# Kernel tuning notes

Hardware: AMD Instinct MI355X
Metric: run time of the kernel (lower is better)

## Reference

```python
import jax, jax.numpy as jnp
import numpy as np
import math

D_MODEL = 512
N_HEAD = 8
HEAD_DIM = D_MODEL // N_HEAD


def _rel_sinusoid(seq_len, dim):
    # Sinusoidal embedding for relative positions -seq_len .. seq_len-1, shape [2L, dim]
    half = dim // 2
    inv_freq = jnp.exp(jnp.arange(half, dtype=jnp.float32) * (-math.log(10000.0) / (half - 1)))
    ang = jnp.arange(-seq_len, seq_len, dtype=jnp.float32)[:, None] * inv_freq[None, :]
    return jnp.concatenate([jnp.sin(ang), jnp.cos(ang)], axis=1)  # [2L, dim]


def _shift(BD):
    # Transformer-XL shift trick: [b, n, L, 2L] -> [b, n, L, L]
    b, n, L, _ = BD.shape
    BD = jnp.concatenate([BD, jnp.zeros((b, n, L, 1), BD.dtype)], axis=-1)  # [b,n,L,2L+1]
    BD = BD.reshape(b, n, -1, L)[:, :, :-1].reshape(b, n, L, -1)  # [b,n,L,2L]
    return BD[:, :, :, L:]


def setup_inputs() -> dict:
    key = jax.random.key(0)
    ks = jax.random.split(key, 6)
    B, L = 8, 1024
    x = jax.random.normal(ks[0], (B, L, D_MODEL), jnp.float32)
    mask = jax.random.randint(ks[1], (B, L), 0, 2).astype(jnp.int32)
    W_qkv = jax.random.normal(ks[2], (D_MODEL, 3 * D_MODEL), jnp.float32) / math.sqrt(D_MODEL)
    r_r_bias = jax.random.normal(ks[3], (N_HEAD, HEAD_DIM), jnp.float32) * 0.1
    r_w_bias = jax.random.normal(ks[4], (N_HEAD, HEAD_DIM), jnp.float32) * 0.1
    w_kr = jax.random.normal(ks[5], (HEAD_DIM, HEAD_DIM), jnp.float32) * 0.1
    return {"x": x, "mask": mask, "W_qkv": W_qkv, "r_r_bias": r_r_bias, "r_w_bias": r_w_bias, "w_kr": w_kr}


def reference(x, mask, W_qkv, r_r_bias, r_w_bias, w_kr):
    B, L, d_model = x.shape
    scale = math.sqrt(HEAD_DIM)
    pos_embed = _rel_sinusoid(L, HEAD_DIM)  # [2L, head_dim]

    qkv = x @ W_qkv  # [B, L, 3*d_model]
    q, k, v = jnp.split(qkv, 3, axis=-1)
    q = q.reshape(B, L, N_HEAD, HEAD_DIM).transpose(0, 2, 1, 3)  # [B, H, L, hd]
    k = k.reshape(B, L, N_HEAD, HEAD_DIM).transpose(0, 2, 1, 3)
    v = v.reshape(B, L, N_HEAD, HEAD_DIM).transpose(0, 2, 1, 3)

    rw_head_q = q + r_r_bias[None, :, None, :]
    AC = jnp.einsum('bnqd,bnkd->bnqk', rw_head_q, k)  # [B,H,L,L]

    rel = pos_embed @ w_kr  # [2L, hd]
    D_ = jnp.einsum('nd,ld->nl', r_w_bias, rel)[None, :, None, :]  # [1,H,1,2L]
    B_ = jnp.einsum('bnqd,ld->bnql', q, rel)  # [B,H,L,2L]
    BD = _shift(B_ + D_)  # [B,H,L,L]

    attn = (AC + BD) / scale
    attn = jnp.where(mask[:, None, None, :] == 0, jnp.float32(1e-9), attn)
    attn = jax.nn.softmax(attn, axis=-1)  # dropout is identity at eval

    out = jnp.einsum('bnqk,bnkd->bnqd', attn, v)  # [B,H,L,hd]
    return out.transpose(0, 2, 1, 3).reshape(B, L, d_model)
```

## Files before the change

### kernel.cpp

```cpp
#include <hip/hip_runtime.h>
#include <hip/hip_bf16.h>
#include <stdint.h>

typedef __bf16 bf16x8 __attribute__((ext_vector_type(8)));
typedef float  f32x4  __attribute__((ext_vector_type(4)));

#define D_MODEL 512
#define N_HEAD  8
#define HD      64
#define L_      1024
#define SCALE   0.125f
#define EXP_NEG8 3.35462628e-4f
#define L2E     1.44269504f
#define NEG8L2E -11.54156036f

__device__ __forceinline__ unsigned short f2bf(float f) {
  unsigned int u = __builtin_bit_cast(unsigned int, f);
  u += 0x7FFFu + ((u >> 16) & 1u);
  return (unsigned short)(u >> 16);
}
__device__ __forceinline__ float bf2f(unsigned short h) {
  unsigned int u = ((unsigned int)h) << 16;
  return __builtin_bit_cast(float, u);
}

__device__ __forceinline__ void gld_lds16(const void* g, void* l) {
  __builtin_amdgcn_global_load_lds(
      (const __attribute__((address_space(1))) void*)g,
      (__attribute__((address_space(3))) void*)l, 16, 0, 0);
}
__device__ __forceinline__ void gld_lds4(const void* g, void* l) {
  __builtin_amdgcn_global_load_lds(
      (const __attribute__((address_space(1))) void*)g,
      (__attribute__((address_space(3))) void*)l, 4, 0, 0);
}

__global__ __launch_bounds__(256) void k_cvt_x(const float* __restrict__ x,
                                               unsigned short* __restrict__ xbf) {
  int t = blockIdx.x * 256 + threadIdx.x;
  const float4* p = reinterpret_cast<const float4*>(x) + (size_t)t * 2;
  float4 a = p[0], b = p[1];
  ushort4 o0 = { f2bf(a.x), f2bf(a.y), f2bf(a.z), f2bf(a.w) };
  ushort4 o1 = { f2bf(b.x), f2bf(b.y), f2bf(b.z), f2bf(b.w) };
  ushort4* q = reinterpret_cast<ushort4*>(xbf) + (size_t)t * 2;
  q[0] = o0; q[1] = o1;
}

__global__ __launch_bounds__(256) void k_cvt_wt(const float* __restrict__ W,
                                                unsigned short* __restrict__ Wt) {
  __shared__ float tile[32][33];
  int kb = blockIdx.x;
  int nb = blockIdx.y;
  int t = threadIdx.x;
  int r = t >> 3, c4 = (t & 7) * 4;
  float4 v = *reinterpret_cast<const float4*>(W + (size_t)(kb * 32 + r) * 1536 + nb * 32 + c4);
  tile[r][c4 + 0] = v.x; tile[r][c4 + 1] = v.y; tile[r][c4 + 2] = v.z; tile[r][c4 + 3] = v.w;
  __syncthreads();
  int a = t >> 3, b4 = (t & 7) * 4;
  ushort4 o = { f2bf(tile[b4 + 0][a]), f2bf(tile[b4 + 1][a]),
                f2bf(tile[b4 + 2][a]), f2bf(tile[b4 + 3][a]) };
  *reinterpret_cast<ushort4*>(Wt + (size_t)(nb * 32 + a) * 512 + kb * 32 + b4) = o;
}

__global__ __launch_bounds__(256) void k_stab(float* __restrict__ SCF,
                                              unsigned short* __restrict__ SBF) {
  int tid = blockIdx.x * 256 + threadIdx.x;
  int l = tid >> 6, d = tid & 63;
  const float kInv = -9.210340371976184f / 31.0f;
  float f = expf((float)(d & 31) * kInv);
  float ang = (float)l * f;
  float v = (d < 32) ? sinf(ang) : cosf(ang);
  SCF[tid] = v;
  SBF[tid] = f2bf(v);
}

__global__ __launch_bounds__(256) void k_wz(const unsigned short* __restrict__ Wt,
                                            const float* __restrict__ wkr,
                                            const float* __restrict__ rwb,
                                            unsigned short* __restrict__ Wzt,
                                            float* __restrict__ CZ) {
  __shared__ float wkrS[64][64];
  __shared__ float panS[64][36];
  int blk = blockIdx.x;
  int h = blk >> 4, kc = blk & 15;
  int t = threadIdx.x;
  for (int i = t; i < 4096; i += 256) wkrS[i >> 6][i & 63] = wkr[i];
  {
    int d = t >> 2, j0 = (t & 3) * 8;
    const unsigned short* src = Wt + (size_t)(h * 64 + d) * 512 + kc * 32 + j0;
    for (int j = 0; j < 8; ++j) panS[d][j0 + j] = bf2f(src[j]);
  }
  __syncthreads();
  int e = t >> 2, j0 = (t & 3) * 8;
  float acc[8];
  for (int j = 0; j < 8; ++j) acc[j] = 0.f;
  for (int d = 0; d < 64; ++d) {
    float wv = wkrS[e][d];
    for (int j = 0; j < 8; ++j) acc[j] += wv * panS[d][j0 + j];
  }
  unsigned short* dst = Wzt + (size_t)(h * 64 + e) * 512 + kc * 32 + j0;
  ushort4 o0 = { f2bf(acc[0]), f2bf(acc[1]), f2bf(acc[2]), f2bf(acc[3]) };
  ushort4 o1 = { f2bf(acc[4]), f2bf(acc[5]), f2bf(acc[6]), f2bf(acc[7]) };
  *reinterpret_cast<ushort4*>(dst) = o0;
  *reinterpret_cast<ushort4*>(dst + 4) = o1;
  if (kc == 0 && t < 64) {
    float c = 0.f;
    for (int d = 0; d < 64; ++d) c += wkrS[t][d] * rwb[h * 64 + d];
    CZ[h * 64 + t] = c;
  }
}

__global__ __launch_bounds__(256, 3) void k_gemm_qkv(const unsigned short* __restrict__ Xbf,
                                                     const unsigned short* __restrict__ Wt,
                                                     const float* __restrict__ rrb,
                                                     const float* __restrict__ SCF,
                                                     const float* __restrict__ CZ,
                                                     unsigned short* __restrict__ QKV,
                                                     unsigned short* __restrict__ Vt,
                                                     unsigned short* __restrict__ Aq) {
  __shared__ unsigned short As[2][128][32];
  __shared__ unsigned short Bs[2][128][32];
  int lin = blockIdx.y * 64 + blockIdx.x;
  int xcd = lin & 7, idx = lin >> 3;
  int bx = xcd * 8 + idx / 16;
  int by = idx % 16;
  int m0 = bx * 128;
  int n0 = by * 128;
  int w = threadIdx.x >> 6, lane = threadIdx.x & 63;
  int lr = lane & 15, g = lane >> 4;
  int wm = (w >> 1) * 64, wn = (w & 1) * 64;
  int srow = lane >> 2, schk = (lane & 3) * 8;

  auto stage = [&](int buf, int k0) {
#pragma unroll
    for (int j = 0; j < 2; ++j) {
      int row = w * 32 + j * 16 + srow;
      gld_lds16(Xbf + (size_t)(m0 + row) * 512 + k0 + schk, &As[buf][w * 32 + j * 16][0]);
      gld_lds16(Wt  + (size_t)(n0 + row) * 512 + k0 + schk, &Bs[buf][w * 32 + j * 16][0]);
    }
  };

  f32x4 acc[4][4];
  for (int i = 0; i < 4; ++i) for (int j = 0; j < 4; ++j) acc[i][j] = (f32x4){0.f, 0.f, 0.f, 0.f};

  stage(0, 0);
  __syncthreads();

  for (int it = 0; it < 16; ++it) {
    int cur = it & 1;
    if (it < 15) stage(cur ^ 1, (it + 1) * 32);
    bf16x8 a[4], b[4];
#pragma unroll
    for (int mt = 0; mt < 4; ++mt)
      a[mt] = __builtin_bit_cast(bf16x8, *reinterpret_cast<const uint4*>(&As[cur][wm + mt * 16 + lr][g * 8]));
#pragma unroll
    for (int nt = 0; nt < 4; ++nt)
      b[nt] = __builtin_bit_cast(bf16x8, *reinterpret_cast<const uint4*>(&Bs[cur][wn + nt * 16 + lr][g * 8]));
#pragma unroll
    for (int mt = 0; mt < 4; ++mt)
#pragma unroll
      for (int nt = 0; nt < 4; ++nt)
        acc[mt][nt] = __builtin_amdgcn_mfma_f32_16x16x32_bf16(a[mt], b[nt], acc[mt][nt], 0, 0, 0);
    __syncthreads();
  }

  int region = n0 >> 9;
  if (region == 3) {
    int nvb = (n0 - 1536) + wn;
    int h = nvb >> 6;
    int bb = m0 >> 10;
    float cz0 = CZ[nvb + lr];
    float cz1 = CZ[nvb + 16 + lr];
    float cz2 = CZ[nvb + 32 + lr];
    float cz3 = CZ[nvb + 48 + lr];
#pragma unroll
    for (int mt = 0; mt < 4; ++mt)
#pragma unroll
      for (int r = 0; r < 4; ++r) {
        int m = m0 + wm + mt * 16 + g * 4 + r;
        int lrow = m & 1023;
        const float* sc = SCF + (size_t)lrow * 64;
        float s0 = sc[lr], s1 = sc[16 + lr], c0 = sc[32 + lr], c1 = sc[48 + lr];
        float z0 = acc[mt][0][r] + cz0;
        float z1 = acc[mt][1][r] + cz1;
        float z2 = acc[mt][2][r] + cz2;
        float z3 = acc[mt][3][r] + cz3;
        unsigned short* ap = Aq + ((size_t)(bb * 8 + h) * 1024 + lrow) * 64;
        ap[lr]      = f2bf((z0 * c0 + z2 * s0) * SCALE);
        ap[16 + lr] = f2bf((z1 * c1 + z3 * s1) * SCALE);
        ap[32 + lr] = f2bf((z2 * c0 - z0 * s0) * SCALE);
        ap[48 + lr] = f2bf((z3 * c1 - z1 * s1) * SCALE);
      }
  } else if (region == 2) {
#pragma unroll
    for (int mt = 0; mt < 4; ++mt)
#pragma unroll
      for (int nt = 0; nt < 4; ++nt) {
        int m = m0 + wm + mt * 16 + g * 4;
        int n = n0 + wn + nt * 16 + lr;
        int nv = n - 1024;
        int bb = m >> 10, h = nv >> 6, d = nv & 63;
        ushort4 o = { f2bf(acc[mt][nt][0]), f2bf(acc[mt][nt][1]),
                      f2bf(acc[mt][nt][2]), f2bf(acc[mt][nt][3]) };
        *reinterpret_cast<ushort4*>(Vt + (size_t)((bb * 8 + h) * 64 + d) * 1024 + (m & 1023)) = o;
      }
  } else if (region == 0) {
#pragma unroll
    for (int mt = 0; mt < 4; ++mt)
#pragma unroll
      for (int nt = 0; nt < 4; ++nt) {
        int n = n0 + wn + nt * 16 + lr;
        float bias = rrb[n];
#pragma unroll
        for (int r = 0; r < 4; ++r) {
          int m = m0 + wm + mt * 16 + g * 4 + r;
          QKV[(size_t)m * 1536 + n] = f2bf((acc[mt][nt][r] + bias) * SCALE);
        }
      }
  } else {
#pragma unroll
    for (int mt = 0; mt < 4; ++mt)
#pragma unroll
      for (int nt = 0; nt < 4; ++nt)
#pragma unroll
        for (int r = 0; r < 4; ++r) {
          int m = m0 + wm + mt * 16 + g * 4 + r;
          int n = n0 + wn + nt * 16 + lr;
          QKV[(size_t)m * 1536 + n] = f2bf(acc[mt][nt][r]);
        }
  }
}

__global__ __launch_bounds__(256, 3) void k_attn(const unsigned short* __restrict__ QKV,
                                                 const unsigned short* __restrict__ Vt,
                                                 const unsigned short* __restrict__ Sbf,
                                                 const unsigned short* __restrict__ Aq,
                                                 const int* __restrict__ mask,
                                                 float* __restrict__ out) {
  __shared__ unsigned short KtS[2][64][64];
  __shared__ unsigned short VtS[2][64][64];
  __shared__ int MtS[2][64];
  __shared__ unsigned short pS[4][32][64];

  int n_ = blockIdx.x;
  int l = (n_ & 7) * 64 + (n_ >> 3);
  int bh = l >> 3, qt = l & 7;
  int b = bh >> 3, h = bh & 7;
  int w = threadIdx.x >> 6, lane = threadIdx.x & 63;
  int lr = lane & 15, g = lane >> 4;
  int qw0 = qt * 128 + w * 32;
  int rsub = lane >> 3;
  int csub = (lane & 7) ^ rsub;
  int swz = lr & 7;

  bf16x8 qrr[2][2], qa[2][2];
#pragma unroll
  for (int mt = 0; mt < 2; ++mt) {
    const unsigned short* qrow = QKV + (size_t)(b * L_ + qw0 + mt * 16 + lr) * 1536 + h * HD;
    const unsigned short* arow = Aq + ((size_t)bh * L_ + qw0 + mt * 16 + lr) * HD;
#pragma unroll
    for (int ks = 0; ks < 2; ++ks) {
      qrr[mt][ks] = __builtin_bit_cast(bf16x8, *reinterpret_cast<const uint4*>(qrow + ks * 32 + g * 8));
      qa[mt][ks]  = __builtin_bit_cast(bf16x8, *reinterpret_cast<const uint4*>(arow + ks * 32 + g * 8));
    }
  }

  auto stage = [&](int nb, int k0n) {
#pragma unroll
    for (int j = 0; j < 2; ++j) {
      int row = w * 16 + j * 8;
      const unsigned short* gK = QKV + (size_t)(b * L_ + k0n + row + rsub) * 1536 +
                                 D_MODEL + h * HD + csub * 8;
      gld_lds16(gK, &KtS[nb][row][0]);
      const unsigned short* gV = Vt + (size_t)(bh * HD + row + rsub) * L_ + k0n + csub * 8;
      gld_lds16(gV, &VtS[nb][row][0]);
    }
    if (w == 0) gld_lds4(mask + b * L_ + k0n + lane, &MtS[nb][0]);
  };

  stage(0, 0);

  float lsum[2] = {0.f, 0.f};
  f32x4 accO[2][4];
#pragma unroll
  for (int mt = 0; mt < 2; ++mt)
#pragma unroll
    for (int nt = 0; nt < 4; ++nt) accO[mt][nt] = (f32x4){0.f, 0.f, 0.f, 0.f};

  char* psw = (char*)&pS[w][0][0];
  __syncthreads();

  for (int it = 0; it < 16; ++it) {
    int k0 = it << 6;
    int cur = it & 1;
    if (it < 15) stage(cur ^ 1, k0 + 64);

    bf16x8 sf[4][2];
#pragma unroll
    for (int t4 = 0; t4 < 4; ++t4)
#pragma unroll
      for (int ks = 0; ks < 2; ++ks)
        sf[t4][ks] = __builtin_bit_cast(bf16x8, *reinterpret_cast<const uint4*>(
            Sbf + (size_t)(k0 + t4 * 16 + lr) * HD + ks * 32 + g * 8));

    f32x4 ac[2][4];
#pragma unroll
    for (int mt = 0; mt < 2; ++mt)
#pragma unroll
      for (int t4 = 0; t4 < 4; ++t4) ac[mt][t4] = (f32x4){0.f, 0.f, 0.f, 0.f};
#pragma unroll
    for (int t4 = 0; t4 < 4; ++t4) {
#pragma unroll
      for (int ks = 0; ks < 2; ++ks) {
        const unsigned short* kp = &KtS[cur][t4 * 16 + lr][((((ks << 2) | g) ^ swz) << 3)];
        bf16x8 kfr = __builtin_bit_cast(bf16x8, *reinterpret_cast<const uint4*>(kp));
        ac[0][t4] = __builtin_amdgcn_mfma_f32_16x16x32_bf16(kfr, qrr[0][ks], ac[0][t4], 0, 0, 0);
        ac[1][t4] = __builtin_amdgcn_mfma_f32_16x16x32_bf16(kfr, qrr[1][ks], ac[1][t4], 0, 0, 0);
      }
#pragma unroll
      for (int ks = 0; ks < 2; ++ks) {
        ac[0][t4] = __builtin_amdgcn_mfma_f32_16x16x32_bf16(sf[t4][ks], qa[0][ks], ac[0][t4], 0, 0, 0);
        ac[1][t4] = __builtin_amdgcn_mfma_f32_16x16x32_bf16(sf[t4][ks], qa[1][ks], ac[1][t4], 0, 0, 0);
      }
    }

#pragma unroll
    for (int t4 = 0; t4 < 4; ++t4) {
      int4 mk = *reinterpret_cast<const int4*>(&MtS[cur][t4 * 16 + g * 4]);
#pragma unroll
      for (int mt = 0; mt < 2; ++mt) {
        float e0 = __builtin_amdgcn_exp2f(fmaf(ac[mt][t4][0], L2E, NEG8L2E));
        float e1 = __builtin_amdgcn_exp2f(fmaf(ac[mt][t4][1], L2E, NEG8L2E));
        float e2 = __builtin_amdgcn_exp2f(fmaf(ac[mt][t4][2], L2E, NEG8L2E));
        float e3 = __builtin_amdgcn_exp2f(fmaf(ac[mt][t4][3], L2E, NEG8L2E));
        e0 = mk.x ? e0 : EXP_NEG8;
        e1 = mk.y ? e1 : EXP_NEG8;
        e2 = mk.z ? e2 : EXP_NEG8;
        e3 = mk.w ? e3 : EXP_NEG8;
        lsum[mt] += (e0 + e1) + (e2 + e3);
        unsigned int lo, hi;
        asm("v_cvt_pk_bf16_f32 %0, %1, %2" : "=v"(lo) : "v"(e0), "v"(e1));
        asm("v_cvt_pk_bf16_f32 %0, %1, %2" : "=v"(hi) : "v"(e2), "v"(e3));
        uint2 pk; pk.x = lo; pk.y = hi;
        *reinterpret_cast<uint2*>(psw + ((mt * 16 + lr) * 128 +
            (((t4 << 5) | (g << 3)) ^ (swz << 4)))) = pk;
      }
    }

    bf16x8 pa[2][2];
#pragma unroll
    for (int mt = 0; mt < 2; ++mt)
#pragma unroll
      for (int ks = 0; ks < 2; ++ks)
        pa[mt][ks] = __builtin_bit_cast(bf16x8, *reinterpret_cast<const uint4*>(
            psw + ((mt * 16 + lr) * 128 + (((ks << 6) | (g << 4)) ^ (swz << 4)))));
#pragma unroll
    for (int nt = 0; nt < 4; ++nt)
#pragma unroll
      for (int ks = 0; ks < 2; ++ks) {
        const unsigned short* vp = &VtS[cur][nt * 16 + lr][((((ks << 2) | g) ^ swz) << 3)];
        bf16x8 vfr = __builtin_bit_cast(bf16x8, *reinterpret_cast<const uint4*>(vp));
        accO[0][nt] = __builtin_amdgcn_mfma_f32_16x16x32_bf16(pa[0][ks], vfr, accO[0][nt], 0, 0, 0);
        accO[1][nt] = __builtin_amdgcn_mfma_f32_16x16x32_bf16(pa[1][ks], vfr, accO[1][nt], 0, 0, 0);
      }
    __syncthreads();
  }

#pragma unroll
  for (int mt = 0; mt < 2; ++mt) {
    lsum[mt] += __shfl_xor(lsum[mt], 16);
    lsum[mt] += __shfl_xor(lsum[mt], 32);
  }
  float dsum[2][4];
#pragma unroll
  for (int mt = 0; mt < 2; ++mt)
#pragma unroll
    for (int r = 0; r < 4; ++r) dsum[mt][r] = __shfl(lsum[mt], g * 4 + r);

#pragma unroll
  for (int mt = 0; mt < 2; ++mt)
#pragma unroll
    for (int nt = 0; nt < 4; ++nt)
#pragma unroll
      for (int r = 0; r < 4; ++r) {
        int q = qw0 + mt * 16 + g * 4 + r;
        out[(size_t)(b * L_ + q) * D_MODEL + h * HD + nt * 16 + lr] = accO[mt][nt][r] / dsum[mt][r];
      }
}

extern "C" void kernel_launch(void* const* d_in, const int* in_sizes, int n_in,
                              void* d_out, int out_size, void* d_ws, size_t ws_size,
                              hipStream_t stream) {
  const float* x    = (const float*)d_in[0];
  const int*   mask = (const int*)d_in[1];
  const float* Wqkv = (const float*)d_in[2];
  const float* rrb  = (const float*)d_in[3];
  const float* rwb  = (const float*)d_in[4];
  const float* wkr  = (const float*)d_in[5];
  float* out = (float*)d_out;

  char* ws = (char*)d_ws;
  size_t off = 0;
  unsigned short* XBF = (unsigned short*)(ws + off); off += (size_t)8192 * 512 * 2;
  unsigned short* WT  = (unsigned short*)(ws + off); off += (size_t)2048 * 512 * 2;
  unsigned short* QKV = (unsigned short*)(ws + off); off += (size_t)8192 * 1536 * 2;
  unsigned short* VT  = (unsigned short*)(ws + off); off += (size_t)64 * 64 * 1024 * 2;
  unsigned short* AQ  = (unsigned short*)(ws + off); off += (size_t)64 * 1024 * 64 * 2;
  float*          SCF = (float*)(ws + off);          off += (size_t)1024 * 64 * 4;
  unsigned short* SBF = (unsigned short*)(ws + off); off += (size_t)1024 * 64 * 2;
  float*          CZ  = (float*)(ws + off);          off += 512 * 4;

  hipLaunchKernelGGL(k_cvt_x,    dim3(2048),   dim3(256), 0, stream, x, XBF);
  hipLaunchKernelGGL(k_cvt_wt,   dim3(16, 48), dim3(256), 0, stream, Wqkv, WT);
  hipLaunchKernelGGL(k_stab,     dim3(256),    dim3(256), 0, stream, SCF, SBF);
  hipLaunchKernelGGL(k_wz,       dim3(128),    dim3(256), 0, stream, WT, wkr, rwb, WT + (size_t)1536 * 512, CZ);
  hipLaunchKernelGGL(k_gemm_qkv, dim3(64, 16), dim3(256), 0, stream, XBF, WT, rrb, SCF, CZ, QKV, VT, AQ);
  hipLaunchKernelGGL(k_attn,     dim3(512),    dim3(256), 0, stream, QKV, VT, SBF, AQ, mask, out);
}
```

Measured before the change: 92.75 us.

## Merge prep kernels into one launch and split attention into smaller blocks

Three preprocessing kernels (weight transpose, sinusoid table, wkr-folded weights) are combined into one launch, with the folded-weight branch reading the fp32 weights directly so it no longer depends on the transposed output. The attention kernel moves from 256-thread blocks covering 128 queries to 128-thread blocks covering 64 queries, doubling the grid, with a new XCD-aware block mapping. The mask is now read from global memory into registers instead of being staged through LDS. This cuts launch overhead and aims to spread attention work more evenly across CUs, at the cost of each block reusing its staged K/V tiles for fewer queries and lower occupancy hints.

Result: slower. 98.93 us (+6.7%).

```diff
diff --git a/kernel.cpp b/kernel.cpp
--- a/kernel.cpp
+++ b/kernel.cpp
@@ -28,11 +28,6 @@
   __builtin_amdgcn_global_load_lds(
       (const __attribute__((address_space(1))) void*)g,
       (__attribute__((address_space(3))) void*)l, 16, 0, 0);
-}
-__device__ __forceinline__ void gld_lds4(const void* g, void* l) {
-  __builtin_amdgcn_global_load_lds(
-      (const __attribute__((address_space(1))) void*)g,
-      (__attribute__((address_space(3))) void*)l, 4, 0, 0);
 }
 
 __global__ __launch_bounds__(256) void k_cvt_x(const float* __restrict__ x,
@@ -46,67 +41,66 @@
   q[0] = o0; q[1] = o1;
 }
 
-__global__ __launch_bounds__(256) void k_cvt_wt(const float* __restrict__ W,
-                                                unsigned short* __restrict__ Wt) {
-  __shared__ float tile[32][33];
-  int kb = blockIdx.x;
-  int nb = blockIdx.y;
+__global__ __launch_bounds__(256) void k_prep(const float* __restrict__ W,
+                                              const float* __restrict__ wkr,
+                                              const float* __restrict__ rwb,
+                                              unsigned short* __restrict__ Wt,
+                                              unsigned short* __restrict__ Wzt,
+                                              float* __restrict__ CZ,
+                                              float* __restrict__ SCF,
+                                              unsigned short* __restrict__ SBF) {
+  __shared__ float shm[6208];
+  int blk = blockIdx.x;
   int t = threadIdx.x;
-  int r = t >> 3, c4 = (t & 7) * 4;
-  float4 v = *reinterpret_cast<const float4*>(W + (size_t)(kb * 32 + r) * 1536 + nb * 32 + c4);
-  tile[r][c4 + 0] = v.x; tile[r][c4 + 1] = v.y; tile[r][c4 + 2] = v.z; tile[r][c4 + 3] = v.w;
-  __syncthreads();
-  int a = t >> 3, b4 = (t & 7) * 4;
-  ushort4 o = { f2bf(tile[b4 + 0][a]), f2bf(tile[b4 + 1][a]),
-                f2bf(tile[b4 + 2][a]), f2bf(tile[b4 + 3][a]) };
-  *reinterpret_cast<ushort4*>(Wt + (size_t)(nb * 32 + a) * 512 + kb * 32 + b4) = o;
-}
-
-__global__ __launch_bounds__(256) void k_stab(float* __restrict__ SCF,
-                                              unsigned short* __restrict__ SBF) {
-  int tid = blockIdx.x * 256 + threadIdx.x;
-  int l = tid >> 6, d = tid & 63;
-  const float kInv = -9.210340371976184f / 31.0f;
-  float f = expf((float)(d & 31) * kInv);
-  float ang = (float)l * f;
-  float v = (d < 32) ? sinf(ang) : cosf(ang);
-  SCF[tid] = v;
-  SBF[tid] = f2bf(v);
-}
-
-__global__ __launch_bounds__(256) void k_wz(const unsigned short* __restrict__ Wt,
-                                            const float* __restrict__ wkr,
-                                            const float* __restrict__ rwb,
-                                            unsigned short* __restrict__ Wzt,
-                                            float* __restrict__ CZ) {
-  __shared__ float wkrS[64][64];
-  __shared__ float panS[64][36];
-  int blk = blockIdx.x;
-  int h = blk >> 4, kc = blk & 15;
-  int t = threadIdx.x;
-  for (int i = t; i < 4096; i += 256) wkrS[i >> 6][i & 63] = wkr[i];
-  {
-    int d = t >> 2, j0 = (t & 3) * 8;
-    const unsigned short* src = Wt + (size_t)(h * 64 + d) * 512 + kc * 32 + j0;
-    for (int j = 0; j < 8; ++j) panS[d][j0 + j] = bf2f(src[j]);
-  }
-  __syncthreads();
-  int e = t >> 2, j0 = (t & 3) * 8;
-  float acc[8];
-  for (int j = 0; j < 8; ++j) acc[j] = 0.f;
-  for (int d = 0; d < 64; ++d) {
-    float wv = wkrS[e][d];
-    for (int j = 0; j < 8; ++j) acc[j] += wv * panS[d][j0 + j];
-  }
-  unsigned short* dst = Wzt + (size_t)(h * 64 + e) * 512 + kc * 32 + j0;
-  ushort4 o0 = { f2bf(acc[0]), f2bf(acc[1]), f2bf(acc[2]), f2bf(acc[3]) };
-  ushort4 o1 = { f2bf(acc[4]), f2bf(acc[5]), f2bf(acc[6]), f2bf(acc[7]) };
-  *reinterpret_cast<ushort4*>(dst) = o0;
-  *reinterpret_cast<ushort4*>(dst + 4) = o1;
-  if (kc == 0 && t < 64) {
-    float c = 0.f;
-    for (int d = 0; d < 64; ++d) c += wkrS[t][d] * rwb[h * 64 + d];
-    CZ[h * 64 + t] = c;
+  if (blk < 768) {
+    float (*tile)[33] = reinterpret_cast<float (*)[33]>(shm);
+    int kb = blk & 15, nb = blk >> 4;
+    int r = t >> 3, c4 = (t & 7) * 4;
+    float4 v = *reinterpret_cast<const float4*>(W + (size_t)(kb * 32 + r) * 1536 + nb * 32 + c4);
+    tile[r][c4 + 0] = v.x; tile[r][c4 + 1] = v.y; tile[r][c4 + 2] = v.z; tile[r][c4 + 3] = v.w;
+    __syncthreads();
+    int a = t >> 3, b4 = (t & 7) * 4;
+    ushort4 o = { f2bf(tile[b4 + 0][a]), f2bf(tile[b4 + 1][a]),
+                  f2bf(tile[b4 + 2][a]), f2bf(tile[b4 + 3][a]) };
+    *reinterpret_cast<ushort4*>(Wt + (size_t)(nb * 32 + a) * 512 + kb * 32 + b4) = o;
+  } else if (blk < 1024) {
+    int tid = (blk - 768) * 256 + t;
+    int l = tid >> 6, d = tid & 63;
+    const float kInv = -9.210340371976184f / 31.0f;
+    float f = expf((float)(d & 31) * kInv);
+    float ang = (float)l * f;
+    float v = (d < 32) ? sinf(ang) : cosf(ang);
+    SCF[tid] = v;
+    SBF[tid] = f2bf(v);
+  } else {
+    int blk2 = blk - 1024;
+    int h = blk2 >> 4, kc = blk2 & 15;
+    float* wkrS = shm;
+    float (*panS)[33] = reinterpret_cast<float (*)[33]>(shm + 4096);
+    for (int i = t; i < 4096; i += 256) wkrS[i] = wkr[i];
+    {
+      int kr = t >> 3, d0 = (t & 7) * 8;
+      const float* src = W + (size_t)(kc * 32 + kr) * 1536 + h * 64 + d0;
+      for (int j = 0; j < 8; ++j) panS[d0 + j][kr] = src[j];
+    }
+    __syncthreads();
+    int e = t >> 2, j0 = (t & 3) * 8;
+    float acc[8];
+    for (int j = 0; j < 8; ++j) acc[j] = 0.f;
+    for (int d = 0; d < 64; ++d) {
+      float wv = wkrS[e * 64 + d];
+      for (int j = 0; j < 8; ++j) acc[j] += wv * panS[d][j0 + j];
+    }
+    unsigned short* dst = Wzt + (size_t)(h * 64 + e) * 512 + kc * 32 + j0;
+    ushort4 o0 = { f2bf(acc[0]), f2bf(acc[1]), f2bf(acc[2]), f2bf(acc[3]) };
+    ushort4 o1 = { f2bf(acc[4]), f2bf(acc[5]), f2bf(acc[6]), f2bf(acc[7]) };
+    *reinterpret_cast<ushort4*>(dst) = o0;
+    *reinterpret_cast<ushort4*>(dst + 4) = o1;
+    if (kc == 0 && t < 64) {
+      float c = 0.f;
+      for (int d = 0; d < 64; ++d) c += wkrS[t * 64 + d] * rwb[h * 64 + d];
+      CZ[h * 64 + t] = c;
+    }
   }
 }
 
@@ -231,7 +225,7 @@
   }
 }
 
-__global__ __launch_bounds__(256, 3) void k_attn(const unsigned short* __restrict__ QKV,
+__global__ __launch_bounds__(128, 2) void k_attn(const unsigned short* __restrict__ QKV,
                                                  const unsigned short* __restrict__ Vt,
                                                  const unsigned short* __restrict__ Sbf,
                                                  const unsigned short* __restrict__ Aq,
@@ -239,16 +233,16 @@
                                                  float* __restrict__ out) {
   __shared__ unsigned short KtS[2][64][64];
   __shared__ unsigned short VtS[2][64][64];
-  __shared__ int MtS[2][64];
-  __shared__ unsigned short pS[4][32][64];
+  __shared__ unsigned short pS[2][32][64];
 
   int n_ = blockIdx.x;
-  int l = (n_ & 7) * 64 + (n_ >> 3);
-  int bh = l >> 3, qt = l & 7;
+  int xcd = n_ & 7, idx = n_ >> 3;
+  int bh = xcd * 8 + (idx >> 4);
+  int qt = idx & 15;
   int b = bh >> 3, h = bh & 7;
   int w = threadIdx.x >> 6, lane = threadIdx.x & 63;
   int lr = lane & 15, g = lane >> 4;
-  int qw0 = qt * 128 + w * 32;
+  int qw0 = qt * 64 + w * 32;
   int rsub = lane >> 3;
   int csub = (lane & 7) ^ rsub;
   int swz = lr & 7;
@@ -267,15 +261,14 @@
 
   auto stage = [&](int nb, int k0n) {
 #pragma unroll
-    for (int j = 0; j < 2; ++j) {
-      int row = w * 16 + j * 8;
+    for (int j = 0; j < 4; ++j) {
+      int row = w * 32 + j * 8;
       const unsigned short* gK = QKV + (size_t)(b * L_ + k0n + row + rsub) * 1536 +
                                  D_MODEL + h * HD + csub * 8;
       gld_lds16(gK, &KtS[nb][row][0]);
       const unsigned short* gV = Vt + (size_t)(bh * HD + row + rsub) * L_ + k0n + csub * 8;
       gld_lds16(gV, &VtS[nb][row][0]);
     }
-    if (w == 0) gld_lds4(mask + b * L_ + k0n + lane, &MtS[nb][0]);
   };
 
   stage(0, 0);
@@ -302,6 +295,11 @@
       for (int ks = 0; ks < 2; ++ks)
         sf[t4][ks] = __builtin_bit_cast(bf16x8, *reinterpret_cast<const uint4*>(
             Sbf + (size_t)(k0 + t4 * 16 + lr) * HD + ks * 32 + g * 8));
+
+    int4 mk[4];
+#pragma unroll
+    for (int t4 = 0; t4 < 4; ++t4)
+      mk[t4] = *reinterpret_cast<const int4*>(mask + b * L_ + k0 + t4 * 16 + g * 4);
 
     f32x4 ac[2][4];
 #pragma unroll
@@ -326,17 +324,16 @@
 
 #pragma unroll
     for (int t4 = 0; t4 < 4; ++t4) {
-      int4 mk = *reinterpret_cast<const int4*>(&MtS[cur][t4 * 16 + g * 4]);
 #pragma unroll
       for (int mt = 0; mt < 2; ++mt) {
         float e0 = __builtin_amdgcn_exp2f(fmaf(ac[mt][t4][0], L2E, NEG8L2E));
         float e1 = __builtin_amdgcn_exp2f(fmaf(ac[mt][t4][1], L2E, NEG8L2E));
         float e2 = __builtin_amdgcn_exp2f(fmaf(ac[mt][t4][2], L2E, NEG8L2E));
         float e3 = __builtin_amdgcn_exp2f(fmaf(ac[mt][t4][3], L2E, NEG8L2E));
-        e0 = mk.x ? e0 : EXP_NEG8;
-        e1 = mk.y ? e1 : EXP_NEG8;
-        e2 = mk.z ? e2 : EXP_NEG8;
-        e3 = mk.w ? e3 : EXP_NEG8;
+        e0 = mk[t4].x ? e0 : EXP_NEG8;
+        e1 = mk[t4].y ? e1 : EXP_NEG8;
+        e2 = mk[t4].z ? e2 : EXP_NEG8;
+        e3 = mk[t4].w ? e3 : EXP_NEG8;
         lsum[mt] += (e0 + e1) + (e2 + e3);
         unsigned int lo, hi;
         asm("v_cvt_pk_bf16_f32 %0, %1, %2" : "=v"(lo) : "v"(e0), "v"(e1));
@@ -411,9 +408,8 @@
   float*          CZ  = (float*)(ws + off);          off += 512 * 4;
 
   hipLaunchKernelGGL(k_cvt_x,    dim3(2048),   dim3(256), 0, stream, x, XBF);
-  hipLaunchKernelGGL(k_cvt_wt,   dim3(16, 48), dim3(256), 0, stream, Wqkv, WT);
-  hipLaunchKernelGGL(k_stab,     dim3(256),    dim3(256), 0, stream, SCF, SBF);
-  hipLaunchKernelGGL(k_wz,       dim3(128),    dim3(256), 0, stream, WT, wkr, rwb, WT + (size_t)1536 * 512, CZ);
+  hipLaunchKernelGGL(k_prep,     dim3(1152),   dim3(256), 0, stream,
+                     Wqkv, wkr, rwb, WT, WT + (size_t)1536 * 512, CZ, SCF, SBF);
   hipLaunchKernelGGL(k_gemm_qkv, dim3(64, 16), dim3(256), 0, stream, XBF, WT, rrb, SCF, CZ, QKV, VT, AQ);
-  hipLaunchKernelGGL(k_attn,     dim3(512),    dim3(256), 0, stream, QKV, VT, SBF, AQ, mask, out);
-}
+  hipLaunchKernelGGL(k_attn,     dim3(1024),   dim3(128), 0, stream, QKV, VT, SBF, AQ, mask, out);
+}
```
